# Optimization experiments

Hardware: AMD Instinct MI355X
Metric: run time of the kernel (lower is better)

## Reference

```python
import jax, jax.numpy as jnp
import numpy as np

B, T, D = 64, 4096, 256
UNITS = 256

def setup_inputs() -> dict:
    key = jax.random.key(0)
    k0, k1, k2, k3 = jax.random.split(key, 4)
    lstm_output = jax.random.normal(k0, (B, T, D), dtype=jnp.float32)
    # Glorot-ish scaled dense weights (no bias per module)
    W1 = jax.random.normal(k1, (D, UNITS), dtype=jnp.float32) * (1.0 / np.sqrt(D))
    W2 = jax.random.normal(k2, (D, UNITS), dtype=jnp.float32) * (1.0 / np.sqrt(D))
    v = jax.random.normal(k3, (UNITS, 1), dtype=jnp.float32) * (1.0 / np.sqrt(UNITS))
    return {"lstm_output": lstm_output, "W1": W1, "W2": W2, "v": v}

def reference(lstm_output, W1, W2, v):
    # query/key: [B, T, units]
    query = jnp.einsum("btd,du->btu", lstm_output, W1)
    key = jnp.einsum("btd,du->btu", lstm_output, W2)
    # score: [B, T, 1]
    score = jnp.einsum("btu,uo->bto", jnp.tanh(query + key), v)
    # softmax over time axis (axis=1)
    attention_weights = jax.nn.softmax(score, axis=1)
    # context: [B, D]
    context_vector = jnp.sum(attention_weights * lstm_output, axis=1)
    return (context_vector, attention_weights)
```

## Files before the change

kernel.cpp:

```cpp
#include <hip/hip_runtime.h>
#include <math.h>

#define B 64
#define T 4096
#define D 256
#define U 256

typedef __attribute__((ext_vector_type(8)))  short s16x8;
typedef __attribute__((ext_vector_type(16))) float f32x16;

#define MT 32
#define SPB 16
#define NBLK ((B*T)/(MT*SPB))
#define LDAP 33

#define DPP_ADD(v, ctrl)                                                     \
  v += __int_as_float(__builtin_amdgcn_update_dpp(                           \
      0, __float_as_int(v), ctrl, 0xF, 0xF, true))

__global__ __launch_bounds__(512, 2) void scores_ctx_kernel(
    const float* __restrict__ A,
    const float* __restrict__ W1,
    const float* __restrict__ W2,
    const float* __restrict__ v,
    float* __restrict__ w_out,
    float* __restrict__ part,
    float* __restrict__ zpart)
{
  __shared__ uint4 AH[32 * LDAP];
  __shared__ uint4 AL[32 * LDAP];
  __shared__ float red[32][8];
  __shared__ float wavebuf[8][16][16];
  __shared__ float zred[8];

  const int tid  = threadIdx.x;
  const int lane = tid & 63;
  const int wv   = tid >> 6;
  const int l31  = lane & 31;
  const int half = lane >> 5;

  const int n = wv * 32 + l31;
  s16x8 Bh[16], Bl[16];
#pragma unroll
  for (int s = 0; s < 16; ++s) {
    s16x8 bh, bl;
#pragma unroll
    for (int j = 0; j < 8; ++j) {
      const int k = s * 16 + half * 8 + j;
      const float w = W1[k * 256 + n] + W2[k * 256 + n];
      const unsigned int uw = __float_as_uint(w);
      const float wl = w - __uint_as_float(uw & 0xffff0000u);
      bh[j] = (short)(uw >> 16);
      bl[j] = (short)(__float_as_uint(wl) >> 16);
    }
    Bh[s] = bh; Bl[s] = bl;
  }
  const float vv = v[n];

  const int sm  = tid >> 4;
  const int sc0 = tid & 15;

  float acc[16];
#pragma unroll
  for (int q = 0; q < 16; ++q) acc[q] = 0.f;
  float zacc = 0.f;

  const size_t row0 = (size_t)blockIdx.x * (MT * SPB);
  float4 rg[4];
  {
    const float4* src = (const float4*)(A + (row0 + sm) * 256);
#pragma unroll
    for (int i = 0; i < 4; ++i) rg[i] = src[sc0 + 16 * i];
  }

  for (int step = 0; step < SPB; ++step) {
    const size_t rowbase = row0 + (size_t)step * MT;

#pragma unroll
    for (int i = 0; i < 4; ++i) {
      const float4 a = rg[i];
      const int k  = 4 * (sc0 + 16 * i);
      const int k8 = k >> 3;
      const int off = (k >> 2) & 1;
      const unsigned int ux = __float_as_uint(a.x), uy = __float_as_uint(a.y);
      const unsigned int uz = __float_as_uint(a.z), uw = __float_as_uint(a.w);
      const uint2 hi2 = make_uint2((ux >> 16) | (uy & 0xffff0000u),
                                   (uz >> 16) | (uw & 0xffff0000u));
      const float lx = a.x - __uint_as_float(ux & 0xffff0000u);
      const float ly = a.y - __uint_as_float(uy & 0xffff0000u);
      const float lz = a.z - __uint_as_float(uz & 0xffff0000u);
      const float lw = a.w - __uint_as_float(uw & 0xffff0000u);
      const uint2 lo2 = make_uint2(
          (__float_as_uint(lx) >> 16) | (__float_as_uint(ly) & 0xffff0000u),
          (__float_as_uint(lz) >> 16) | (__float_as_uint(lw) & 0xffff0000u));
      ((uint2*)&AH[k8 * LDAP + sm])[off] = hi2;
      ((uint2*)&AL[k8 * LDAP + sm])[off] = lo2;
    }
    __syncthreads();

    float4 rgc[4];
#pragma unroll
    for (int i = 0; i < 4; ++i) rgc[i] = rg[i];

    if (step + 1 < SPB) {
      const float4* src = (const float4*)(A + (rowbase + MT + sm) * 256);
#pragma unroll
      for (int i = 0; i < 4; ++i) rg[i] = src[sc0 + 16 * i];
    }

    f32x16 a0 = {}, a1 = {};
#pragma unroll
    for (int s = 0; s < 16; ++s) {
      const uint4 qh = AH[(2 * s + half) * LDAP + l31];
      const uint4 ql = AL[(2 * s + half) * LDAP + l31];
      const s16x8 ah = __builtin_bit_cast(s16x8, qh);
      const s16x8 al = __builtin_bit_cast(s16x8, ql);
      a0 = __builtin_amdgcn_mfma_f32_32x32x16_bf16(ah, Bh[s], a0, 0, 0, 0);
      a1 = __builtin_amdgcn_mfma_f32_32x32x16_bf16(ah, Bl[s], a1, 0, 0, 0);
      a1 = __builtin_amdgcn_mfma_f32_32x32x16_bf16(al, Bh[s], a1, 0, 0, 0);
    }

#pragma unroll
    for (int r = 0; r < 16; ++r) {
      const float x = a0[r] + a1[r];
      const float e = __expf(x + x);
      float p = (1.f - 2.f * __builtin_amdgcn_rcpf(e + 1.f)) * vv;
      DPP_ADD(p, 0xB1);
      DPP_ADD(p, 0x4E);
      DPP_ADD(p, 0x141);
      DPP_ADD(p, 0x140);
      p += __int_as_float(
          __builtin_amdgcn_ds_swizzle(__float_as_int(p), 0x401F));
      if (l31 == 0)
        red[(r & 3) + 8 * (r >> 2) + 4 * half][wv] = p;
    }
    __syncthreads();

    {
      const float4* rp = (const float4*)&red[sm][0];
      const float4 ra = rp[0], rb = rp[1];
      const float s8 =
          ra.x + ra.y + ra.z + ra.w + rb.x + rb.y + rb.z + rb.w;
      const float w = __expf(s8);
      if (sc0 == 0) {
        w_out[rowbase + sm] = w;
        zacc += w;
      }
#pragma unroll
      for (int i = 0; i < 4; ++i) {
        acc[4 * i + 0] = fmaf(w, rgc[i].x, acc[4 * i + 0]);
        acc[4 * i + 1] = fmaf(w, rgc[i].y, acc[4 * i + 1]);
        acc[4 * i + 2] = fmaf(w, rgc[i].z, acc[4 * i + 2]);
        acc[4 * i + 3] = fmaf(w, rgc[i].w, acc[4 * i + 3]);
      }
    }
  }

#pragma unroll
  for (int q = 0; q < 16; ++q) {
    float p = acc[q];
    p += __shfl_xor(p, 16);
    p += __shfl_xor(p, 32);
    acc[q] = p;
  }
  if (lane < 16) {
#pragma unroll
    for (int q = 0; q < 16; ++q) wavebuf[wv][lane][q] = acc[q];
  }
  {
    float z = zacc;
    z += __shfl_xor(z, 16);
    z += __shfl_xor(z, 32);
    if (lane == 0) zred[wv] = z;
  }
  __syncthreads();

  if (tid < 256) {
    const int sc = (tid & 63) >> 2;
    const int q  = 4 * (tid >> 6) + (tid & 3);
    float ssum = 0.f;
#pragma unroll
    for (int wvi = 0; wvi < 8; ++wvi) ssum += wavebuf[wvi][sc][q];
    part[blockIdx.x * 256 + tid] = ssum;
  }
  if (tid == 0) {
    float zz = 0.f;
#pragma unroll
    for (int i = 0; i < 8; ++i) zz += zred[i];
    zpart[blockIdx.x] = zz;
  }
}

__global__ __launch_bounds__(1024) void finalize_kernel(
    const float* __restrict__ part,
    const float* __restrict__ zpart,
    float* __restrict__ attn,
    float* __restrict__ ctx)
{
  const int b = blockIdx.x;
  const int tid = threadIdx.x;
  __shared__ float shinv;
  if (tid == 0) {
    float z = 0.f;
#pragma unroll
    for (int c = 0; c < 8; ++c) z += zpart[b * 8 + c];
    shinv = 1.0f / z;
  }
  __syncthreads();
  const float iz = shinv;

  if (tid < D) {
    float s = 0.f;
#pragma unroll
    for (int c = 0; c < 8; ++c) s += part[(b * 8 + c) * D + tid];
    ctx[b * D + tid] = s * iz;
  }

  float4* row = (float4*)(attn + (long)b * T);
  float4 w4 = row[tid];
  w4.x *= iz; w4.y *= iz; w4.z *= iz; w4.w *= iz;
  row[tid] = w4;
}

extern "C" void kernel_launch(void* const* d_in, const int* in_sizes, int n_in,
                              void* d_out, int out_size, void* d_ws, size_t ws_size,
                              hipStream_t stream) {
    const float* lstm = (const float*)d_in[0];
    const float* W1   = (const float*)d_in[1];
    const float* W2   = (const float*)d_in[2];
    const float* v    = (const float*)d_in[3];

    float* out  = (float*)d_out;
    float* ctx  = out;
    float* attn = out + B * D;

    float* part  = (float*)d_ws;
    float* zpart = part + NBLK * D;

    scores_ctx_kernel<<<NBLK, 512, 0, stream>>>(lstm, W1, W2, v, attn, part, zpart);
    finalize_kernel<<<B, 1024, 0, stream>>>(part, zpart, attn, ctx);
}
```

Measured before the change: 397.0 us.

## Triple-buffer LDS tiles and defer weighted context accumulation one step

Staging of the A tile moves into a three-slot LDS ring, with global prefetch two steps ahead. The exp/weighted-context accumulation for step i-1 is deferred to overlap with step i's MFMA work, so each step needs one barrier instead of two. Rows per block are doubled, which halves the block count, and finalize now reduces the matching number of partials. The context now multiplies by the bf16 high half read from LDS instead of the full fp32 values, which cuts register pressure but loses precision in the context output.

```diff
diff --git a/kernel.cpp b/kernel.cpp
--- a/kernel.cpp
+++ b/kernel.cpp
@@ -10,13 +10,60 @@
 typedef __attribute__((ext_vector_type(16))) float f32x16;
 
 #define MT 32
-#define SPB 16
+#define SPB 32
 #define NBLK ((B*T)/(MT*SPB))
 #define LDAP 33
 
 #define DPP_ADD(v, ctrl)                                                     \
   v += __int_as_float(__builtin_amdgcn_update_dpp(                           \
       0, __float_as_int(v), ctrl, 0xF, 0xF, true))
+
+__device__ __forceinline__ void stage_tile(uint4* bufH, uint4* bufL,
+                                           const float4* rg, int sm, int sc0) {
+#pragma unroll
+  for (int i = 0; i < 4; ++i) {
+    const float4 a = rg[i];
+    const int k  = 4 * (sc0 + 16 * i);
+    const int k8 = k >> 3;
+    const int off = (k >> 2) & 1;
+    const unsigned int ux = __float_as_uint(a.x), uy = __float_as_uint(a.y);
+    const unsigned int uz = __float_as_uint(a.z), uw = __float_as_uint(a.w);
+    const uint2 hi2 = make_uint2((ux >> 16) | (uy & 0xffff0000u),
+                                 (uz >> 16) | (uw & 0xffff0000u));
+    const float lx = a.x - __uint_as_float(ux & 0xffff0000u);
+    const float ly = a.y - __uint_as_float(uy & 0xffff0000u);
+    const float lz = a.z - __uint_as_float(uz & 0xffff0000u);
+    const float lw = a.w - __uint_as_float(uw & 0xffff0000u);
+    const uint2 lo2 = make_uint2(
+        (__float_as_uint(lx) >> 16) | (__float_as_uint(ly) & 0xffff0000u),
+        (__float_as_uint(lz) >> 16) | (__float_as_uint(lw) & 0xffff0000u));
+    ((uint2*)&bufH[k8 * LDAP + sm])[off] = hi2;
+    ((uint2*)&bufL[k8 * LDAP + sm])[off] = lo2;
+  }
+}
+
+__device__ __forceinline__ void wctx_accum(
+    const float (*redp)[8], const uint4* bufH, size_t rowb,
+    int sm, int sc0, float* __restrict__ w_out, float* acc, float& zacc) {
+  const float4* rp = (const float4*)&redp[sm][0];
+  const float4 ra = rp[0], rb = rp[1];
+  const float s8 = ra.x + ra.y + ra.z + ra.w + rb.x + rb.y + rb.z + rb.w;
+  const float w = __expf(s8);
+  if (sc0 == 0) { w_out[rowb + sm] = w; zacc += w; }
+#pragma unroll
+  for (int i = 0; i < 4; ++i) {
+    const int c = sc0 + 16 * i;
+    const uint2 h = ((const uint2*)&bufH[(c >> 1) * LDAP + sm])[c & 1];
+    const float x0 = __uint_as_float(h.x << 16);
+    const float x1 = __uint_as_float(h.x & 0xffff0000u);
+    const float x2 = __uint_as_float(h.y << 16);
+    const float x3 = __uint_as_float(h.y & 0xffff0000u);
+    acc[4 * i + 0] = fmaf(w, x0, acc[4 * i + 0]);
+    acc[4 * i + 1] = fmaf(w, x1, acc[4 * i + 1]);
+    acc[4 * i + 2] = fmaf(w, x2, acc[4 * i + 2]);
+    acc[4 * i + 3] = fmaf(w, x3, acc[4 * i + 3]);
+  }
+}
 
 __global__ __launch_bounds__(512, 2) void scores_ctx_kernel(
     const float* __restrict__ A,
@@ -27,9 +74,9 @@
     float* __restrict__ part,
     float* __restrict__ zpart)
 {
-  __shared__ uint4 AH[32 * LDAP];
-  __shared__ uint4 AL[32 * LDAP];
-  __shared__ float red[32][8];
+  __shared__ uint4 AH3[3][32 * LDAP];
+  __shared__ uint4 AL3[3][32 * LDAP];
+  __shared__ float red[2][32][8];
   __shared__ float wavebuf[8][16][16];
   __shared__ float zred[8];
 
@@ -72,47 +119,50 @@
 #pragma unroll
     for (int i = 0; i < 4; ++i) rg[i] = src[sc0 + 16 * i];
   }
-
+  stage_tile(AH3[0], AL3[0], rg, sm, sc0);
+  {
+    const float4* src = (const float4*)(A + (row0 + MT + sm) * 256);
+#pragma unroll
+    for (int i = 0; i < 4; ++i) rg[i] = src[sc0 + 16 * i];
+  }
+  __syncthreads();
+
+  int cur = 0;
   for (int step = 0; step < SPB; ++step) {
-    const size_t rowbase = row0 + (size_t)step * MT;
-
-#pragma unroll
-    for (int i = 0; i < 4; ++i) {
-      const float4 a = rg[i];
-      const int k  = 4 * (sc0 + 16 * i);
-      const int k8 = k >> 3;
-      const int off = (k >> 2) & 1;
-      const unsigned int ux = __float_as_uint(a.x), uy = __float_as_uint(a.y);
-      const unsigned int uz = __float_as_uint(a.z), uw = __float_as_uint(a.w);
-      const uint2 hi2 = make_uint2((ux >> 16) | (uy & 0xffff0000u),
-                                   (uz >> 16) | (uw & 0xffff0000u));
-      const float lx = a.x - __uint_as_float(ux & 0xffff0000u);
-      const float ly = a.y - __uint_as_float(uy & 0xffff0000u);
-      const float lz = a.z - __uint_as_float(uz & 0xffff0000u);
-      const float lw = a.w - __uint_as_float(uw & 0xffff0000u);
-      const uint2 lo2 = make_uint2(
-          (__float_as_uint(lx) >> 16) | (__float_as_uint(ly) & 0xffff0000u),
-          (__float_as_uint(lz) >> 16) | (__float_as_uint(lw) & 0xffff0000u));
-      ((uint2*)&AH[k8 * LDAP + sm])[off] = hi2;
-      ((uint2*)&AL[k8 * LDAP + sm])[off] = lo2;
-    }
-    __syncthreads();
-
-    float4 rgc[4];
-#pragma unroll
-    for (int i = 0; i < 4; ++i) rgc[i] = rg[i];
-
-    if (step + 1 < SPB) {
-      const float4* src = (const float4*)(A + (rowbase + MT + sm) * 256);
+    const int nxt = (cur == 2) ? 0 : cur + 1;
+    const int prv = (nxt == 2) ? 0 : nxt + 1;
+    const int par = step & 1;
+
+    if (step > 0)
+      wctx_accum(red[par ^ 1], AH3[prv], row0 + (size_t)(step - 1) * MT,
+                 sm, sc0, w_out, acc, zacc);
+
+    f32x16 a0 = {}, a1 = {};
+    const uint4* cH = AH3[cur];
+    const uint4* cL = AL3[cur];
+#pragma unroll
+    for (int s = 0; s < 8; ++s) {
+      const uint4 qh = cH[(2 * s + half) * LDAP + l31];
+      const uint4 ql = cL[(2 * s + half) * LDAP + l31];
+      const s16x8 ah = __builtin_bit_cast(s16x8, qh);
+      const s16x8 al = __builtin_bit_cast(s16x8, ql);
+      a0 = __builtin_amdgcn_mfma_f32_32x32x16_bf16(ah, Bh[s], a0, 0, 0, 0);
+      a1 = __builtin_amdgcn_mfma_f32_32x32x16_bf16(ah, Bl[s], a1, 0, 0, 0);
+      a1 = __builtin_amdgcn_mfma_f32_32x32x16_bf16(al, Bh[s], a1, 0, 0, 0);
+    }
+
+    if (step + 1 < SPB) stage_tile(AH3[nxt], AL3[nxt], rg, sm, sc0);
+    if (step + 2 < SPB) {
+      const float4* src =
+          (const float4*)(A + (row0 + (size_t)(step + 2) * MT + sm) * 256);
 #pragma unroll
       for (int i = 0; i < 4; ++i) rg[i] = src[sc0 + 16 * i];
     }
 
-    f32x16 a0 = {}, a1 = {};
-#pragma unroll
-    for (int s = 0; s < 16; ++s) {
-      const uint4 qh = AH[(2 * s + half) * LDAP + l31];
-      const uint4 ql = AL[(2 * s + half) * LDAP + l31];
+#pragma unroll
+    for (int s = 8; s < 16; ++s) {
+      const uint4 qh = cH[(2 * s + half) * LDAP + l31];
+      const uint4 ql = cL[(2 * s + half) * LDAP + l31];
       const s16x8 ah = __builtin_bit_cast(s16x8, qh);
       const s16x8 al = __builtin_bit_cast(s16x8, ql);
       a0 = __builtin_amdgcn_mfma_f32_32x32x16_bf16(ah, Bh[s], a0, 0, 0, 0);
@@ -132,29 +182,14 @@
       p += __int_as_float(
           __builtin_amdgcn_ds_swizzle(__float_as_int(p), 0x401F));
       if (l31 == 0)
-        red[(r & 3) + 8 * (r >> 2) + 4 * half][wv] = p;
+        red[par][(r & 3) + 8 * (r >> 2) + 4 * half][wv] = p;
     }
     __syncthreads();
-
-    {
-      const float4* rp = (const float4*)&red[sm][0];
-      const float4 ra = rp[0], rb = rp[1];
-      const float s8 =
-          ra.x + ra.y + ra.z + ra.w + rb.x + rb.y + rb.z + rb.w;
-      const float w = __expf(s8);
-      if (sc0 == 0) {
-        w_out[rowbase + sm] = w;
-        zacc += w;
-      }
-#pragma unroll
-      for (int i = 0; i < 4; ++i) {
-        acc[4 * i + 0] = fmaf(w, rgc[i].x, acc[4 * i + 0]);
-        acc[4 * i + 1] = fmaf(w, rgc[i].y, acc[4 * i + 1]);
-        acc[4 * i + 2] = fmaf(w, rgc[i].z, acc[4 * i + 2]);
-        acc[4 * i + 3] = fmaf(w, rgc[i].w, acc[4 * i + 3]);
-      }
-    }
-  }
+    cur = nxt;
+  }
+
+  wctx_accum(red[(SPB - 1) & 1], AH3[(SPB - 1) % 3],
+             row0 + (size_t)(SPB - 1) * MT, sm, sc0, w_out, acc, zacc);
 
 #pragma unroll
   for (int q = 0; q < 16; ++q) {
@@ -191,6 +226,7 @@
   }
 }
 
+#define BPB (NBLK / B)
 __global__ __launch_bounds__(1024) void finalize_kernel(
     const float* __restrict__ part,
     const float* __restrict__ zpart,
@@ -203,7 +239,7 @@
   if (tid == 0) {
     float z = 0.f;
 #pragma unroll
-    for (int c = 0; c < 8; ++c) z += zpart[b * 8 + c];
+    for (int c = 0; c < BPB; ++c) z += zpart[b * BPB + c];
     shinv = 1.0f / z;
   }
   __syncthreads();
@@ -212,7 +248,7 @@
   if (tid < D) {
     float s = 0.f;
 #pragma unroll
-    for (int c = 0; c < 8; ++c) s += part[(b * 8 + c) * D + tid];
+    for (int c = 0; c < BPB; ++c) s += part[(b * BPB + c) * D + tid];
     ctx[b * D + tid] = s * iz;
   }
 
```

Result: slower. 406.7 us (+2.4%).

## Double-buffer LDS tiles, switch to 16x16x32 MFMA with 1024-thread blocks

Applied to the files above, without the earlier changes.

Moves the fused scores/context kernel to 1024-thread blocks of 16 waves, each owning 16 output units through 16x16x32 bf16 MFMAs. The A tile is double-buffered in LDS so staging of the next tile overlaps the current matrix multiply, leaving one barrier per step instead of two. The softmax-weighted context accumulation is deferred by one step and re-reads A from global memory (probably L2) rather than keeping it in registers. Blocks now process 32 steps, halving the grid, and the finalize kernel adapts to the new number of partials per batch. The risks are the extra global re-reads, the 1024-thread occupancy target, and fewer, larger blocks.

```diff
diff --git a/kernel.cpp b/kernel.cpp
--- a/kernel.cpp
+++ b/kernel.cpp
@@ -6,19 +6,38 @@
 #define D 256
 #define U 256
 
-typedef __attribute__((ext_vector_type(8)))  short s16x8;
-typedef __attribute__((ext_vector_type(16))) float f32x16;
+typedef __attribute__((ext_vector_type(8))) short s16x8;
+typedef __attribute__((ext_vector_type(4))) float f32x4;
 
 #define MT 32
-#define SPB 16
+#define SPB 32
 #define NBLK ((B*T)/(MT*SPB))
-#define LDAP 33
+#define RQ 33
 
 #define DPP_ADD(v, ctrl)                                                     \
   v += __int_as_float(__builtin_amdgcn_update_dpp(                           \
       0, __float_as_int(v), ctrl, 0xF, 0xF, true))
 
-__global__ __launch_bounds__(512, 2) void scores_ctx_kernel(
+__device__ __forceinline__ void stage16(uint4* bufH, uint4* bufL,
+                                        const float4* rg, int rowg, int c8) {
+  uint4 hi, lo;
+  unsigned* hp = (unsigned*)&hi;
+  unsigned* lp = (unsigned*)&lo;
+  const float* f = (const float*)rg;
+#pragma unroll
+  for (int jw = 0; jw < 4; ++jw) {
+    const unsigned u0 = __float_as_uint(f[2 * jw]);
+    const unsigned u1 = __float_as_uint(f[2 * jw + 1]);
+    hp[jw] = (u0 >> 16) | (u1 & 0xffff0000u);
+    const float l0 = f[2 * jw]     - __uint_as_float(u0 & 0xffff0000u);
+    const float l1 = f[2 * jw + 1] - __uint_as_float(u1 & 0xffff0000u);
+    lp[jw] = (__float_as_uint(l0) >> 16) | (__float_as_uint(l1) & 0xffff0000u);
+  }
+  bufH[rowg * RQ + c8] = hi;
+  bufL[rowg * RQ + c8] = lo;
+}
+
+__global__ __launch_bounds__(1024, 4) void scores_ctx_kernel(
     const float* __restrict__ A,
     const float* __restrict__ W1,
     const float* __restrict__ W2,
@@ -27,28 +46,28 @@
     float* __restrict__ part,
     float* __restrict__ zpart)
 {
-  __shared__ uint4 AH[32 * LDAP];
-  __shared__ uint4 AL[32 * LDAP];
-  __shared__ float red[32][8];
-  __shared__ float wavebuf[8][16][16];
-  __shared__ float zred[8];
+  __shared__ uint4 tiles[4][32 * RQ];
+  __shared__ float red[2][32][16];
+  __shared__ float zw[32];
 
   const int tid  = threadIdx.x;
   const int lane = tid & 63;
   const int wv   = tid >> 6;
-  const int l31  = lane & 31;
-  const int half = lane >> 5;
-
-  const int n = wv * 32 + l31;
-  s16x8 Bh[16], Bl[16];
-#pragma unroll
-  for (int s = 0; s < 16; ++s) {
+  const int l15  = lane & 15;
+  const int g4   = lane >> 4;
+  const int rowg = tid >> 5;
+  const int c8   = tid & 31;
+
+  const int n = wv * 16 + l15;
+  s16x8 Bh[8], Bl[8];
+#pragma unroll
+  for (int s = 0; s < 8; ++s) {
     s16x8 bh, bl;
 #pragma unroll
     for (int j = 0; j < 8; ++j) {
-      const int k = s * 16 + half * 8 + j;
+      const int k = s * 32 + g4 * 8 + j;
       const float w = W1[k * 256 + n] + W2[k * 256 + n];
-      const unsigned int uw = __float_as_uint(w);
+      const unsigned uw = __float_as_uint(w);
       const float wl = w - __uint_as_float(uw & 0xffff0000u);
       bh[j] = (short)(uw >> 16);
       bl[j] = (short)(__float_as_uint(wl) >> 16);
@@ -57,140 +76,133 @@
   }
   const float vv = v[n];
 
-  const int sm  = tid >> 4;
-  const int sc0 = tid & 15;
-
-  float acc[16];
-#pragma unroll
-  for (int q = 0; q < 16; ++q) acc[q] = 0.f;
+  float acc[8] = {0.f, 0.f, 0.f, 0.f, 0.f, 0.f, 0.f, 0.f};
   float zacc = 0.f;
 
   const size_t row0 = (size_t)blockIdx.x * (MT * SPB);
-  float4 rg[4];
+  float4 rg[2];
   {
-    const float4* src = (const float4*)(A + (row0 + sm) * 256);
-#pragma unroll
-    for (int i = 0; i < 4; ++i) rg[i] = src[sc0 + 16 * i];
-  }
-
+    const float4* src = (const float4*)(A + (row0 + rowg) * 256 + c8 * 8);
+    rg[0] = src[0]; rg[1] = src[1];
+  }
+  stage16(tiles[0], tiles[1], rg, rowg, c8);
+  {
+    const float4* src = (const float4*)(A + (row0 + MT + rowg) * 256 + c8 * 8);
+    rg[0] = src[0]; rg[1] = src[1];
+  }
+  __syncthreads();
+
+  int cur = 0;
   for (int step = 0; step < SPB; ++step) {
-    const size_t rowbase = row0 + (size_t)step * MT;
-
-#pragma unroll
-    for (int i = 0; i < 4; ++i) {
-      const float4 a = rg[i];
-      const int k  = 4 * (sc0 + 16 * i);
-      const int k8 = k >> 3;
-      const int off = (k >> 2) & 1;
-      const unsigned int ux = __float_as_uint(a.x), uy = __float_as_uint(a.y);
-      const unsigned int uz = __float_as_uint(a.z), uw = __float_as_uint(a.w);
-      const uint2 hi2 = make_uint2((ux >> 16) | (uy & 0xffff0000u),
-                                   (uz >> 16) | (uw & 0xffff0000u));
-      const float lx = a.x - __uint_as_float(ux & 0xffff0000u);
-      const float ly = a.y - __uint_as_float(uy & 0xffff0000u);
-      const float lz = a.z - __uint_as_float(uz & 0xffff0000u);
-      const float lw = a.w - __uint_as_float(uw & 0xffff0000u);
-      const uint2 lo2 = make_uint2(
-          (__float_as_uint(lx) >> 16) | (__float_as_uint(ly) & 0xffff0000u),
-          (__float_as_uint(lz) >> 16) | (__float_as_uint(lw) & 0xffff0000u));
-      ((uint2*)&AH[k8 * LDAP + sm])[off] = hi2;
-      ((uint2*)&AL[k8 * LDAP + sm])[off] = lo2;
+    const int par = step & 1;
+
+    if (step > 0) {
+      const size_t rowb = row0 + (size_t)(step - 1) * MT;
+      const float4* rp = (const float4*)&red[par ^ 1][rowg][0];
+      const float4 q0 = rp[0], q1 = rp[1], q2 = rp[2], q3 = rp[3];
+      const float s8 = ((q0.x + q0.y) + (q0.z + q0.w)) +
+                       ((q1.x + q1.y) + (q1.z + q1.w)) +
+                       ((q2.x + q2.y) + (q2.z + q2.w)) +
+                       ((q3.x + q3.y) + (q3.z + q3.w));
+      const float w = __expf(s8);
+      if (c8 == 0) { w_out[rowb + rowg] = w; zacc += w; }
+      const float4* src = (const float4*)(A + (rowb + rowg) * 256 + c8 * 8);
+      const float4 xa = src[0], xb = src[1];
+      acc[0] = fmaf(w, xa.x, acc[0]); acc[1] = fmaf(w, xa.y, acc[1]);
+      acc[2] = fmaf(w, xa.z, acc[2]); acc[3] = fmaf(w, xa.w, acc[3]);
+      acc[4] = fmaf(w, xb.x, acc[4]); acc[5] = fmaf(w, xb.y, acc[5]);
+      acc[6] = fmaf(w, xb.z, acc[6]); acc[7] = fmaf(w, xb.w, acc[7]);
+    }
+
+    f32x4 dd[2] = {};
+    {
+      const uint4* cH = tiles[cur * 2];
+      const uint4* cL = tiles[cur * 2 + 1];
+#pragma unroll
+      for (int s = 0; s < 8; ++s) {
+        const int ci = s * 4 + g4;
+        const uint4 qh0 = cH[l15 * RQ + ci];
+        const uint4 ql0 = cL[l15 * RQ + ci];
+        const uint4 qh1 = cH[(l15 + 16) * RQ + ci];
+        const uint4 ql1 = cL[(l15 + 16) * RQ + ci];
+        const s16x8 ah0 = __builtin_bit_cast(s16x8, qh0);
+        const s16x8 al0 = __builtin_bit_cast(s16x8, ql0);
+        const s16x8 ah1 = __builtin_bit_cast(s16x8, qh1);
+        const s16x8 al1 = __builtin_bit_cast(s16x8, ql1);
+        dd[0] = __builtin_amdgcn_mfma_f32_16x16x32_bf16(ah0, Bh[s], dd[0], 0, 0, 0);
+        dd[1] = __builtin_amdgcn_mfma_f32_16x16x32_bf16(ah1, Bh[s], dd[1], 0, 0, 0);
+        dd[0] = __builtin_amdgcn_mfma_f32_16x16x32_bf16(ah0, Bl[s], dd[0], 0, 0, 0);
+        dd[1] = __builtin_amdgcn_mfma_f32_16x16x32_bf16(ah1, Bl[s], dd[1], 0, 0, 0);
+        dd[0] = __builtin_amdgcn_mfma_f32_16x16x32_bf16(al0, Bh[s], dd[0], 0, 0, 0);
+        dd[1] = __builtin_amdgcn_mfma_f32_16x16x32_bf16(al1, Bh[s], dd[1], 0, 0, 0);
+      }
+    }
+
+    if (step + 1 < SPB)
+      stage16(tiles[(cur ^ 1) * 2], tiles[(cur ^ 1) * 2 + 1], rg, rowg, c8);
+    if (step + 2 < SPB) {
+      const float4* src =
+          (const float4*)(A + (row0 + (size_t)(step + 2) * MT + rowg) * 256 + c8 * 8);
+      rg[0] = src[0]; rg[1] = src[1];
+    }
+
+#pragma unroll
+    for (int t = 0; t < 2; ++t) {
+#pragma unroll
+      for (int r = 0; r < 4; ++r) {
+        const float x = dd[t][r];
+        const float e = __expf(x + x);
+        float p = (1.f - 2.f * __builtin_amdgcn_rcpf(e + 1.f)) * vv;
+        DPP_ADD(p, 0xB1);
+        DPP_ADD(p, 0x4E);
+        DPP_ADD(p, 0x141);
+        DPP_ADD(p, 0x140);
+        if (l15 == 0) red[par][16 * t + 4 * g4 + r][wv] = p;
+      }
     }
     __syncthreads();
-
-    float4 rgc[4];
-#pragma unroll
-    for (int i = 0; i < 4; ++i) rgc[i] = rg[i];
-
-    if (step + 1 < SPB) {
-      const float4* src = (const float4*)(A + (rowbase + MT + sm) * 256);
-#pragma unroll
-      for (int i = 0; i < 4; ++i) rg[i] = src[sc0 + 16 * i];
-    }
-
-    f32x16 a0 = {}, a1 = {};
-#pragma unroll
-    for (int s = 0; s < 16; ++s) {
-      const uint4 qh = AH[(2 * s + half) * LDAP + l31];
-      const uint4 ql = AL[(2 * s + half) * LDAP + l31];
-      const s16x8 ah = __builtin_bit_cast(s16x8, qh);
-      const s16x8 al = __builtin_bit_cast(s16x8, ql);
-      a0 = __builtin_amdgcn_mfma_f32_32x32x16_bf16(ah, Bh[s], a0, 0, 0, 0);
-      a1 = __builtin_amdgcn_mfma_f32_32x32x16_bf16(ah, Bl[s], a1, 0, 0, 0);
-      a1 = __builtin_amdgcn_mfma_f32_32x32x16_bf16(al, Bh[s], a1, 0, 0, 0);
-    }
-
-#pragma unroll
-    for (int r = 0; r < 16; ++r) {
-      const float x = a0[r] + a1[r];
-      const float e = __expf(x + x);
-      float p = (1.f - 2.f * __builtin_amdgcn_rcpf(e + 1.f)) * vv;
-      DPP_ADD(p, 0xB1);
-      DPP_ADD(p, 0x4E);
-      DPP_ADD(p, 0x141);
-      DPP_ADD(p, 0x140);
-      p += __int_as_float(
-          __builtin_amdgcn_ds_swizzle(__float_as_int(p), 0x401F));
-      if (l31 == 0)
-        red[(r & 3) + 8 * (r >> 2) + 4 * half][wv] = p;
-    }
-    __syncthreads();
-
-    {
-      const float4* rp = (const float4*)&red[sm][0];
-      const float4 ra = rp[0], rb = rp[1];
-      const float s8 =
-          ra.x + ra.y + ra.z + ra.w + rb.x + rb.y + rb.z + rb.w;
-      const float w = __expf(s8);
-      if (sc0 == 0) {
-        w_out[rowbase + sm] = w;
-        zacc += w;
-      }
-#pragma unroll
-      for (int i = 0; i < 4; ++i) {
-        acc[4 * i + 0] = fmaf(w, rgc[i].x, acc[4 * i + 0]);
-        acc[4 * i + 1] = fmaf(w, rgc[i].y, acc[4 * i + 1]);
-        acc[4 * i + 2] = fmaf(w, rgc[i].z, acc[4 * i + 2]);
-        acc[4 * i + 3] = fmaf(w, rgc[i].w, acc[4 * i + 3]);
-      }
-    }
-  }
-
-#pragma unroll
-  for (int q = 0; q < 16; ++q) {
-    float p = acc[q];
-    p += __shfl_xor(p, 16);
-    p += __shfl_xor(p, 32);
-    acc[q] = p;
-  }
-  if (lane < 16) {
-#pragma unroll
-    for (int q = 0; q < 16; ++q) wavebuf[wv][lane][q] = acc[q];
-  }
+    cur ^= 1;
+  }
+
   {
-    float z = zacc;
-    z += __shfl_xor(z, 16);
-    z += __shfl_xor(z, 32);
-    if (lane == 0) zred[wv] = z;
-  }
+    const size_t rowb = row0 + (size_t)(SPB - 1) * MT;
+    const float4* rp = (const float4*)&red[(SPB - 1) & 1][rowg][0];
+    const float4 q0 = rp[0], q1 = rp[1], q2 = rp[2], q3 = rp[3];
+    const float s8 = ((q0.x + q0.y) + (q0.z + q0.w)) +
+                     ((q1.x + q1.y) + (q1.z + q1.w)) +
+                     ((q2.x + q2.y) + (q2.z + q2.w)) +
+                     ((q3.x + q3.y) + (q3.z + q3.w));
+    const float w = __expf(s8);
+    if (c8 == 0) { w_out[rowb + rowg] = w; zacc += w; }
+    const float4* src = (const float4*)(A + (rowb + rowg) * 256 + c8 * 8);
+    const float4 xa = src[0], xb = src[1];
+    acc[0] = fmaf(w, xa.x, acc[0]); acc[1] = fmaf(w, xa.y, acc[1]);
+    acc[2] = fmaf(w, xa.z, acc[2]); acc[3] = fmaf(w, xa.w, acc[3]);
+    acc[4] = fmaf(w, xb.x, acc[4]); acc[5] = fmaf(w, xb.y, acc[5]);
+    acc[6] = fmaf(w, xb.z, acc[6]); acc[7] = fmaf(w, xb.w, acc[7]);
+  }
+
+  float* wb = (float*)&tiles[0][0];
+#pragma unroll
+  for (int j = 0; j < 8; ++j) wb[rowg * 256 + c8 * 8 + j] = acc[j];
+  if (c8 == 0) zw[rowg] = zacc;
   __syncthreads();
 
   if (tid < 256) {
-    const int sc = (tid & 63) >> 2;
-    const int q  = 4 * (tid >> 6) + (tid & 3);
     float ssum = 0.f;
 #pragma unroll
-    for (int wvi = 0; wvi < 8; ++wvi) ssum += wavebuf[wvi][sc][q];
+    for (int g = 0; g < 32; ++g) ssum += wb[g * 256 + tid];
     part[blockIdx.x * 256 + tid] = ssum;
   }
   if (tid == 0) {
-    float zz = 0.f;
-#pragma unroll
-    for (int i = 0; i < 8; ++i) zz += zred[i];
-    zpart[blockIdx.x] = zz;
-  }
-}
-
+    float z = 0.f;
+#pragma unroll
+    for (int i = 0; i < 32; ++i) z += zw[i];
+    zpart[blockIdx.x] = z;
+  }
+}
+
+#define BPB (NBLK / B)
 __global__ __launch_bounds__(1024) void finalize_kernel(
     const float* __restrict__ part,
     const float* __restrict__ zpart,
@@ -203,7 +215,7 @@
   if (tid == 0) {
     float z = 0.f;
 #pragma unroll
-    for (int c = 0; c < 8; ++c) z += zpart[b * 8 + c];
+    for (int c = 0; c < BPB; ++c) z += zpart[b * BPB + c];
     shinv = 1.0f / z;
   }
   __syncthreads();
@@ -212,7 +224,7 @@
   if (tid < D) {
     float s = 0.f;
 #pragma unroll
-    for (int c = 0; c < 8; ++c) s += part[(b * 8 + c) * D + tid];
+    for (int c = 0; c < BPB; ++c) s += part[(b * BPB + c) * D + tid];
     ctx[b * D + tid] = s * iz;
   }
 
@@ -237,6 +249,6 @@
     float* part  = (float*)d_ws;
     float* zpart = part + NBLK * D;
 
-    scores_ctx_kernel<<<NBLK, 512, 0, stream>>>(lstm, W1, W2, v, attn, part, zpart);
+    scores_ctx_kernel<<<NBLK, 1024, 0, stream>>>(lstm, W1, W2, v, attn, part, zpart);
     finalize_kernel<<<B, 1024, 0, stream>>>(part, zpart, attn, ctx);
 }
```

Measured after the change: 460.4 us. +16.0%, slower.
